# Performance work log

Hardware: AMD Instinct MI355X
Metric: run time of the kernel (lower is better)

## Reference

```python
import jax, jax.numpy as jnp
import numpy as np

B, T, C, HS = 8, 2048, 1024, 64

def setup_inputs() -> dict:
    key = jax.random.key(0)
    ks = jax.random.split(key, 6)
    return {
        "q_vec": jax.random.normal(ks[0], (B, T, C), dtype=jnp.float32),
        "k_vec": jax.random.normal(ks[1], (B, T, C), dtype=jnp.float32),
        "v_vec": jax.random.normal(ks[2], (B, T, C), dtype=jnp.float32),
        "mask": jnp.ones((B, T), dtype=jnp.int32),
        "Wq": jax.random.normal(ks[3], (C, HS), dtype=jnp.float32) * (C ** -0.5),
        "Wk": jax.random.normal(ks[4], (C, HS), dtype=jnp.float32) * (C ** -0.5),
        "Wv": jax.random.normal(ks[5], (C, HS), dtype=jnp.float32) * (C ** -0.5),
    }

def reference(q_vec, k_vec, v_vec, mask, Wq, Wk, Wv):
    # bias-free linear projections: [B,T,C] @ [C,HS] -> [B,T,HS]
    q = jnp.einsum('btc,ch->bth', q_vec, Wq)
    k = jnp.einsum('btc,ch->bth', k_vec, Wk)
    v = jnp.einsum('btc,ch->bth', v_vec, Wv)
    scale = k.shape[-1] ** -0.5
    # full T x T score matrix, as in the original module
    scores = jnp.einsum('bth,bsh->bts', q, k) * scale  # [B,T,T]
    Tq = scores.shape[1]
    # _expand_along_time: expanded[b,i,j] = mask[b,j], then causal tril
    mask_exp = jnp.broadcast_to(mask[:, None, :].astype(jnp.float32), scores.shape)
    tril = jnp.tril(jnp.ones((Tq, Tq), dtype=jnp.float32))
    combined = mask_exp * tril[None, :, :]
    scores = jnp.where(combined == 0, -jnp.inf, scores)
    attn = jax.nn.softmax(scores, axis=-1)
    # dropout p=0.0 (eval) -> identity
    out = jnp.einsum('bts,bsh->bth', attn, v)  # [B,T,HS]
    return out
```

## Files before the change

### kernel.cpp

```cpp
#include <hip/hip_runtime.h>
#include <hip/hip_bf16.h>
#include <cmath>
#include <stdint.h>

#define B_ 8
#define T_ 2048
#define C_ 1024
#define HS_ 64
#define NS 8
#define LP 72

typedef __attribute__((ext_vector_type(8))) short short8;
typedef __attribute__((ext_vector_type(4))) float floatx4;

__device__ inline unsigned short f2bf(float f) {
    union { float f; unsigned u; } v; v.f = f;
    unsigned r = v.u + 0x7FFF + ((v.u >> 16) & 1);
    return (unsigned short)(r >> 16);
}
__device__ inline unsigned pk2bf(float a, float b) {
    union { __hip_bfloat162 h; unsigned u; } v;
    v.h = __float22bfloat162_rn(float2{a, b});
    return v.u;
}
__device__ inline float bf2f(unsigned short u) {
    union { unsigned u; float f; } w; w.u = ((unsigned)u) << 16; return w.f;
}

__global__ __launch_bounds__(256) void prep_wt(const float* __restrict__ Wq,
                                               const float* __restrict__ Wk,
                                               const float* __restrict__ Wv,
                                               unsigned short* __restrict__ wf) {
    int p   = blockIdx.x >> 4;
    int blk = blockIdx.x & 15;
    const float* W = (p == 0) ? Wq : (p == 1) ? Wk : Wv;
    unsigned short* Wf = wf + p * 65536;
    #pragma unroll
    for (int it = 0; it < 16; ++it) {
        int idx = blk * 4096 + it * 256 + threadIdx.x;
        int k = idx >> 6, col = idx & 63;
        int ks = k >> 5, quad = (k >> 3) & 3, j = k & 7;
        int nt = col >> 4, l16 = col & 15;
        Wf[(ks * 256 + nt * 64 + quad * 16 + l16) * 8 + j] = f2bf(W[idx]);
    }
}

__global__ __launch_bounds__(256, 6) void proj_kernel(
    const float* __restrict__ qv, const float* __restrict__ kv, const float* __restrict__ vv,
    const unsigned short* __restrict__ wf,
    unsigned short* __restrict__ qb, unsigned short* __restrict__ kb, unsigned short* __restrict__ vb)
{
    __shared__ float rlds[3][16][68];

    const int tid  = threadIdx.x;
    const int wave = tid >> 6, lane = tid & 63, quad = lane >> 4, l16 = lane & 15;
    const int p    = blockIdx.x >> 10;
    const int tile = blockIdx.x & 1023;

    const float* X = (p == 0) ? qv : (p == 1) ? kv : vv;
    unsigned short* Ob = (p == 0) ? qb : (p == 1) ? kb : vb;
    const unsigned short* Wf = wf + p * 65536;
    const float oscale = (p == 0) ? 0.125f : 1.0f;

    const float* xp = X + ((long)tile * 16 + l16) * C_ + wave * 256 + quad * 8;
    const unsigned short* wp = Wf + (wave * 8) * 4 * 512 + lane * 8;

    floatx4 acc[4] = { {0,0,0,0},{0,0,0,0},{0,0,0,0},{0,0,0,0} };

    floatx4 xq[2][2];
    short8  wq[2][4];
    xq[0][0] = *(const floatx4*)(xp);
    xq[0][1] = *(const floatx4*)(xp + 4);
    xq[1][0] = *(const floatx4*)(xp + 32);
    xq[1][1] = *(const floatx4*)(xp + 36);
    #pragma unroll
    for (int nt = 0; nt < 4; ++nt) wq[0][nt] = *(const short8*)(wp + nt * 512);
    #pragma unroll
    for (int nt = 0; nt < 4; ++nt) wq[1][nt] = *(const short8*)(wp + (4 + nt) * 512);

    #pragma unroll
    for (int s = 0; s < 8; ++s) {
        const int bi = s & 1;
        floatx4 ca = xq[bi][0], cb = xq[bi][1];
        short8 b0 = wq[bi][0], b1 = wq[bi][1], b2 = wq[bi][2], b3 = wq[bi][3];

        if (s + 2 < 8) {
            xq[bi][0] = *(const floatx4*)(xp + (s + 2) * 32);
            xq[bi][1] = *(const floatx4*)(xp + (s + 2) * 32 + 4);
            #pragma unroll
            for (int nt = 0; nt < 4; ++nt)
                wq[bi][nt] = *(const short8*)(wp + ((s + 2) * 4 + nt) * 512);
        }

        union { short8 s8; unsigned u[4]; } af;
        af.u[0] = pk2bf(ca[0], ca[1]);
        af.u[1] = pk2bf(ca[2], ca[3]);
        af.u[2] = pk2bf(cb[0], cb[1]);
        af.u[3] = pk2bf(cb[2], cb[3]);

        acc[0] = __builtin_amdgcn_mfma_f32_16x16x32_bf16(af.s8, b0, acc[0], 0, 0, 0);
        acc[1] = __builtin_amdgcn_mfma_f32_16x16x32_bf16(af.s8, b1, acc[1], 0, 0, 0);
        acc[2] = __builtin_amdgcn_mfma_f32_16x16x32_bf16(af.s8, b2, acc[2], 0, 0, 0);
        acc[3] = __builtin_amdgcn_mfma_f32_16x16x32_bf16(af.s8, b3, acc[3], 0, 0, 0);
    }

    if (wave) {
        #pragma unroll
        for (int nt = 0; nt < 4; ++nt)
            #pragma unroll
            for (int r = 0; r < 4; ++r)
                rlds[wave - 1][quad * 4 + r][nt * 16 + l16] = acc[nt][r];
    }
    __syncthreads();
    if (wave == 0) {
        #pragma unroll
        for (int nt = 0; nt < 4; ++nt)
            #pragma unroll
            for (int r = 0; r < 4; ++r)
                acc[nt][r] += rlds[0][quad * 4 + r][nt * 16 + l16]
                            + rlds[1][quad * 4 + r][nt * 16 + l16]
                            + rlds[2][quad * 4 + r][nt * 16 + l16];

        unsigned short* op = Ob + ((long)tile * 16 + quad * 4) * HS_ + l16;
        #pragma unroll
        for (int nt = 0; nt < 4; ++nt)
            #pragma unroll
            for (int r = 0; r < 4; ++r)
                op[r * HS_ + nt * 16] = f2bf(acc[nt][r] * oscale);
    }
}

__global__ __launch_bounds__(256) void attn_partial(
    const unsigned short* __restrict__ qb, const unsigned short* __restrict__ kb,
    const unsigned short* __restrict__ vb, const int* __restrict__ mask,
    unsigned short* __restrict__ Opart, float* __restrict__ Mpart, float* __restrict__ Lpart)
{
    const int s  = blockIdx.x & (NS - 1);
    const int bq = blockIdx.x >> 3;
    const int qt = bq & 31;
    const int b  = bq >> 5;
    if (s > qt) return;

    __shared__ unsigned short Klds[64 * LP];
    __shared__ unsigned short Vt[64 * LP];
    __shared__ unsigned short Plds[4][16 * LP];

    const int tid = threadIdx.x;
    const int wave = tid >> 6, lane = tid & 63, quad = lane >> 4, l16 = lane & 15;

    const int qrow = qt * 64 + wave * 16 + l16;
    const unsigned short* qp = qb + ((long)(b * T_ + qrow)) * HS_;
    short8 aq0 = *(const short8*)&qp[0  + quad * 8];
    short8 aq1 = *(const short8*)&qp[32 + quad * 8];

    floatx4 acc_o[4] = { {0,0,0,0},{0,0,0,0},{0,0,0,0},{0,0,0,0} };
    float m_r[4] = { -INFINITY, -INFINITY, -INFINITY, -INFINITY };
    float l_r[4] = { 0.f, 0.f, 0.f, 0.f };

    const int rowg = qt * 64 + wave * 16 + quad * 4;

    const int skey = tid >> 3;
    const int sf8  = (tid & 7) * 8;
    const int vp = tid & 31, vg = tid >> 5;

    for (int c = s; c <= qt; c += NS) {
        const int kc = c * 64;
        #pragma unroll
        for (int it = 0; it < 2; ++it) {
            int key = it * 32 + skey;
            *(short8*)&Klds[key * LP + sf8] =
                *(const short8*)&kb[((long)(b * T_ + kc + key)) * HS_ + sf8];
        }
        {
            const unsigned short* v0p = &vb[((long)(b * T_ + kc + 2 * vp)) * HS_ + vg * 8];
            short8 v0 = *(const short8*)v0p;
            short8 v1 = *(const short8*)(v0p + HS_);
            #pragma unroll
            for (int j = 0; j < 8; ++j) {
                unsigned pr = (unsigned)(unsigned short)v0[j] |
                              ((unsigned)(unsigned short)v1[j] << 16);
                *(unsigned*)&Vt[(vg * 8 + j) * LP + 2 * vp] = pr;
            }
        }
        __syncthreads();

        floatx4 sv[4];
        #pragma unroll
        for (int kt = 0; kt < 4; ++kt) {
            floatx4 a = {0.f, 0.f, 0.f, 0.f};
            short8 bk0 = *(short8*)&Klds[(kt * 16 + l16) * LP + 0  + quad * 8];
            short8 bk1 = *(short8*)&Klds[(kt * 16 + l16) * LP + 32 + quad * 8];
            a = __builtin_amdgcn_mfma_f32_16x16x32_bf16(aq0, bk0, a, 0, 0, 0);
            a = __builtin_amdgcn_mfma_f32_16x16x32_bf16(aq1, bk1, a, 0, 0, 0);
            sv[kt] = a;
        }

        const bool lastc = (c == qt);
        #pragma unroll
        for (int kt = 0; kt < 4; ++kt) {
            int key = kc + kt * 16 + l16;
            int mk = mask[b * T_ + key];
            #pragma unroll
            for (int r = 0; r < 4; ++r) {
                bool dead = (mk == 0) || (lastc && key > rowg + r);
                if (dead) sv[kt][r] = -INFINITY;
            }
        }

        float alpha[4];
        #pragma unroll
        for (int r = 0; r < 4; ++r) {
            float mx = fmaxf(fmaxf(sv[0][r], sv[1][r]), fmaxf(sv[2][r], sv[3][r]));
            #pragma unroll
            for (int off = 1; off < 16; off <<= 1)
                mx = fmaxf(mx, __shfl_xor(mx, off));
            float mn = fmaxf(m_r[r], mx);
            float a_ = __expf(m_r[r] - mn);
            float ps = 0.f;
            #pragma unroll
            for (int kt = 0; kt < 4; ++kt) {
                float pv = __expf(sv[kt][r] - mn);
                sv[kt][r] = pv;
                ps += pv;
            }
            #pragma unroll
            for (int off = 1; off < 16; off <<= 1)
                ps += __shfl_xor(ps, off);
            l_r[r] = l_r[r] * a_ + ps;
            m_r[r] = mn;
            alpha[r] = a_;
        }
        #pragma unroll
        for (int nt = 0; nt < 4; ++nt)
            #pragma unroll
            for (int r = 0; r < 4; ++r)
                acc_o[nt][r] *= alpha[r];

        unsigned short* pl = Plds[wave];
        #pragma unroll
        for (int kt = 0; kt < 4; ++kt)
            #pragma unroll
            for (int r = 0; r < 4; ++r)
                pl[(quad * 4 + r) * LP + kt * 16 + l16] = f2bf(sv[kt][r]);
        short8 ap0 = *(short8*)&pl[l16 * LP + 0  + quad * 8];
        short8 ap1 = *(short8*)&pl[l16 * LP + 32 + quad * 8];

        #pragma unroll
        for (int nt = 0; nt < 4; ++nt) {
            short8 bv0 = *(short8*)&Vt[(nt * 16 + l16) * LP + 0  + quad * 8];
            short8 bv1 = *(short8*)&Vt[(nt * 16 + l16) * LP + 32 + quad * 8];
            acc_o[nt] = __builtin_amdgcn_mfma_f32_16x16x32_bf16(ap0, bv0, acc_o[nt], 0, 0, 0);
            acc_o[nt] = __builtin_amdgcn_mfma_f32_16x16x32_bf16(ap1, bv1, acc_o[nt], 0, 0, 0);
        }
        __syncthreads();
    }

    unsigned short* Op = Opart + (long)blockIdx.x * 4096;
    #pragma unroll
    for (int nt = 0; nt < 4; ++nt)
        #pragma unroll
        for (int r = 0; r < 4; ++r)
            Op[(wave * 16 + quad * 4 + r) * 64 + nt * 16 + l16] = f2bf(acc_o[nt][r]);
    if (l16 == 0) {
        #pragma unroll
        for (int r = 0; r < 4; ++r) {
            int rl = wave * 16 + quad * 4 + r;
            Mpart[(long)blockIdx.x * 64 + rl] = m_r[r];
            Lpart[(long)blockIdx.x * 64 + rl] = l_r[r];
        }
    }
}

__global__ __launch_bounds__(256) void attn_combine(
    const unsigned short* __restrict__ Opart, const float* __restrict__ Mpart,
    const float* __restrict__ Lpart, float* __restrict__ out)
{
    const int half = blockIdx.x & 1;
    const int bq = blockIdx.x >> 1;
    const int qt = bq & 31;
    const int b  = bq >> 5;
    const int nsp = (qt + 1 < NS) ? qt + 1 : NS;

    const int row  = (threadIdx.x >> 3) + half * 32;
    const int colg = (threadIdx.x & 7) * 8;
    const long base = (long)bq * NS;

    float M = -INFINITY;
    #pragma unroll
    for (int sp = 0; sp < NS; ++sp)
        if (sp < nsp) M = fmaxf(M, Mpart[(base + sp) * 64 + row]);

    float w[NS];
    float L = 0.f;
    #pragma unroll
    for (int sp = 0; sp < NS; ++sp)
        if (sp < nsp) {
            float e = __expf(Mpart[(base + sp) * 64 + row] - M);
            w[sp] = e;
            L += e * Lpart[(base + sp) * 64 + row];
        }

    float acc[8] = {0,0,0,0,0,0,0,0};
    #pragma unroll
    for (int sp = 0; sp < NS; ++sp)
        if (sp < nsp) {
            const unsigned short* Op = Opart + (base + sp) * 4096 + row * 64 + colg;
            short8 o = *(const short8*)Op;
            float ws = w[sp];
            #pragma unroll
            for (int j = 0; j < 8; ++j)
                acc[j] += ws * bf2f((unsigned short)o[j]);
        }

    float inv = 1.0f / L;
    float* op = out + ((long)(b * T_ + qt * 64 + row)) * HS_ + colg;
    floatx4 o0 = { acc[0] * inv, acc[1] * inv, acc[2] * inv, acc[3] * inv };
    floatx4 o1 = { acc[4] * inv, acc[5] * inv, acc[6] * inv, acc[7] * inv };
    *(floatx4*)op = o0;
    *(floatx4*)(op + 4) = o1;
}

extern "C" void kernel_launch(void* const* d_in, const int* in_sizes, int n_in,
                              void* d_out, int out_size, void* d_ws, size_t ws_size,
                              hipStream_t stream)
{
    const float* qv = (const float*)d_in[0];
    const float* kv = (const float*)d_in[1];
    const float* vv = (const float*)d_in[2];
    const int*   mask = (const int*)d_in[3];
    const float* Wq = (const float*)d_in[4];
    const float* Wk = (const float*)d_in[5];
    const float* Wv = (const float*)d_in[6];
    float* out = (float*)d_out;

    unsigned short* wf    = (unsigned short*)d_ws;
    unsigned short* qbuf  = wf + 3 * C_ * HS_;
    unsigned short* kbuf  = qbuf + (long)B_ * T_ * HS_;
    unsigned short* vbuf  = kbuf + (long)B_ * T_ * HS_;
    unsigned short* Opart = vbuf + (long)B_ * T_ * HS_;
    float* Mpart = (float*)(Opart + (long)B_ * 32 * NS * 4096);
    float* Lpart = Mpart + (long)B_ * 32 * NS * 64;

    prep_wt<<<48, 256, 0, stream>>>(Wq, Wk, Wv, wf);
    proj_kernel<<<3072, 256, 0, stream>>>(qv, kv, vv, wf, qbuf, kbuf, vbuf);
    attn_partial<<<B_ * 32 * NS, 256, 0, stream>>>(qbuf, kbuf, vbuf, mask, Opart, Mpart, Lpart);
    attn_combine<<<B_ * 32 * 2, 256, 0, stream>>>(Opart, Mpart, Lpart, out);
}
```

Baseline: 252.1 us.

## Stage X tile in LDS as bf16 with coalesced loads in projection kernel

The projection kernel now loads the 16x1024 fp32 input tile cooperatively, with each thread reading contiguous float4s across rows. It converts the values to bf16 once and stores them in a padded LDS buffer, and the MFMA loop reads its A fragments from LDS. The old per-lane strided global loads, which were software-prefetched, are replaced by fully coalesced reads. The cost is about 33 KB of extra LDS per block, a block-wide barrier before compute, and the dropped occupancy hint in launch bounds, so fewer blocks may fit per CU and load latency is no longer overlapped with MFMA work.

```diff
diff --git a/kernel.cpp b/kernel.cpp
--- a/kernel.cpp
+++ b/kernel.cpp
@@ -9,6 +9,7 @@
 #define HS_ 64
 #define NS 8
 #define LP 72
+#define XLS 1032
 
 typedef __attribute__((ext_vector_type(8))) short short8;
 typedef __attribute__((ext_vector_type(4))) float floatx4;
@@ -45,11 +46,12 @@
     }
 }
 
-__global__ __launch_bounds__(256, 6) void proj_kernel(
+__global__ __launch_bounds__(256) void proj_kernel(
     const float* __restrict__ qv, const float* __restrict__ kv, const float* __restrict__ vv,
     const unsigned short* __restrict__ wf,
     unsigned short* __restrict__ qb, unsigned short* __restrict__ kb, unsigned short* __restrict__ vb)
 {
+    __shared__ unsigned short Xl[16 * XLS];
     __shared__ float rlds[3][16][68];
 
     const int tid  = threadIdx.x;
@@ -62,17 +64,28 @@
     const unsigned short* Wf = wf + p * 65536;
     const float oscale = (p == 0) ? 0.125f : 1.0f;
 
-    const float* xp = X + ((long)tile * 16 + l16) * C_ + wave * 256 + quad * 8;
+    const float* Xt = X + (long)tile * 16 * C_;
+    #pragma unroll
+    for (int g = 0; g < 2; ++g) {
+        floatx4 xv[8];
+        #pragma unroll
+        for (int i = 0; i < 8; ++i)
+            xv[i] = *(const floatx4*)(Xt + (g * 8 + i) * 1024 + tid * 4);
+        #pragma unroll
+        for (int i = 0; i < 8; ++i) {
+            unsigned u0 = pk2bf(xv[i][0], xv[i][1]);
+            unsigned u1 = pk2bf(xv[i][2], xv[i][3]);
+            unsigned* d = (unsigned*)&Xl[(g * 8 + i) * XLS + tid * 4];
+            d[0] = u0; d[1] = u1;
+        }
+    }
+    __syncthreads();
+
     const unsigned short* wp = Wf + (wave * 8) * 4 * 512 + lane * 8;
 
     floatx4 acc[4] = { {0,0,0,0},{0,0,0,0},{0,0,0,0},{0,0,0,0} };
 
-    floatx4 xq[2][2];
-    short8  wq[2][4];
-    xq[0][0] = *(const floatx4*)(xp);
-    xq[0][1] = *(const floatx4*)(xp + 4);
-    xq[1][0] = *(const floatx4*)(xp + 32);
-    xq[1][1] = *(const floatx4*)(xp + 36);
+    short8 wq[2][4];
     #pragma unroll
     for (int nt = 0; nt < 4; ++nt) wq[0][nt] = *(const short8*)(wp + nt * 512);
     #pragma unroll
@@ -81,27 +94,18 @@
     #pragma unroll
     for (int s = 0; s < 8; ++s) {
         const int bi = s & 1;
-        floatx4 ca = xq[bi][0], cb = xq[bi][1];
         short8 b0 = wq[bi][0], b1 = wq[bi][1], b2 = wq[bi][2], b3 = wq[bi][3];
-
         if (s + 2 < 8) {
-            xq[bi][0] = *(const floatx4*)(xp + (s + 2) * 32);
-            xq[bi][1] = *(const floatx4*)(xp + (s + 2) * 32 + 4);
             #pragma unroll
             for (int nt = 0; nt < 4; ++nt)
                 wq[bi][nt] = *(const short8*)(wp + ((s + 2) * 4 + nt) * 512);
         }
-
-        union { short8 s8; unsigned u[4]; } af;
-        af.u[0] = pk2bf(ca[0], ca[1]);
-        af.u[1] = pk2bf(ca[2], ca[3]);
-        af.u[2] = pk2bf(cb[0], cb[1]);
-        af.u[3] = pk2bf(cb[2], cb[3]);
-
-        acc[0] = __builtin_amdgcn_mfma_f32_16x16x32_bf16(af.s8, b0, acc[0], 0, 0, 0);
-        acc[1] = __builtin_amdgcn_mfma_f32_16x16x32_bf16(af.s8, b1, acc[1], 0, 0, 0);
-        acc[2] = __builtin_amdgcn_mfma_f32_16x16x32_bf16(af.s8, b2, acc[2], 0, 0, 0);
-        acc[3] = __builtin_amdgcn_mfma_f32_16x16x32_bf16(af.s8, b3, acc[3], 0, 0, 0);
+        short8 af = *(const short8*)&Xl[l16 * XLS + wave * 256 + s * 32 + quad * 8];
+
+        acc[0] = __builtin_amdgcn_mfma_f32_16x16x32_bf16(af, b0, acc[0], 0, 0, 0);
+        acc[1] = __builtin_amdgcn_mfma_f32_16x16x32_bf16(af, b1, acc[1], 0, 0, 0);
+        acc[2] = __builtin_amdgcn_mfma_f32_16x16x32_bf16(af, b2, acc[2], 0, 0, 0);
+        acc[3] = __builtin_amdgcn_mfma_f32_16x16x32_bf16(af, b3, acc[3], 0, 0, 0);
     }
 
     if (wave) {
```

Result: no change. 250.4 us (-0.7%).
